# Kernel tuning notes

Measured on AMD Instinct MI355X. Metric: run time of the kernel, lower is better.

The kernel has to match this reference:

```python
import jax, jax.numpy as jnp
import numpy as np

B, L_IN, T = 1024, 512, 96
IN_DIM, OUT_DIM = 1, 1
H_ENC, H_DEC = 128, 256  # decoder hidden = 2 * encoder hidden (bidir concat)


def _lstm_cell(x, h, c, Wih, Whh, b):
    # PyTorch gate order: i, f, g, o. b = b_ih + b_hh (equivalent to two biases).
    gates = x @ Wih.T + h @ Whh.T + b
    i, f, g, o = jnp.split(gates, 4, axis=-1)
    c = jax.nn.sigmoid(f) * c + jax.nn.sigmoid(i) * jnp.tanh(g)
    h = jax.nn.sigmoid(o) * jnp.tanh(c)
    return h, c


def _lstm_final(xs, Wih, Whh, b, hidden, reverse=False):
    # xs: [L, B, D]; returns final (h, c) only (encoder outputs are unused).
    h0 = jnp.zeros((xs.shape[1], hidden), xs.dtype)
    c0 = jnp.zeros((xs.shape[1], hidden), xs.dtype)

    def step(carry, x):
        h, c = _lstm_cell(x, carry[0], carry[1], Wih, Whh, b)
        return (h, c), None

    (h, c), _ = jax.lax.scan(step, (h0, c0), xs, reverse=reverse)
    return h, c


def setup_inputs() -> dict:
    key = jax.random.key(0)
    ks = jax.random.split(key, 13)
    p = lambda k, s: (jax.random.normal(k, s, jnp.float32) * 0.05)
    return {
        "source": jax.random.normal(ks[0], (B, L_IN, IN_DIM), jnp.float32),
        "target_tensor": jnp.zeros((B, T, OUT_DIM), jnp.float32),
        "enc_Wih_f": p(ks[1], (4 * H_ENC, IN_DIM)),
        "enc_Whh_f": p(ks[2], (4 * H_ENC, H_ENC)),
        "enc_b_f": p(ks[3], (4 * H_ENC,)),
        "enc_Wih_b": p(ks[4], (4 * H_ENC, IN_DIM)),
        "enc_Whh_b": p(ks[5], (4 * H_ENC, H_ENC)),
        "enc_b_b": p(ks[6], (4 * H_ENC,)),
        "dec_Wih": p(ks[7], (4 * H_DEC, OUT_DIM)),
        "dec_Whh": p(ks[8], (4 * H_DEC, H_DEC)),
        "dec_b": p(ks[9], (4 * H_DEC,)),
        "out_W": p(ks[10], (OUT_DIM, H_DEC)),
        "out_b": p(ks[11], (OUT_DIM,)),
    }


def reference(source, target_tensor, enc_Wih_f, enc_Whh_f, enc_b_f,
              enc_Wih_b, enc_Whh_b, enc_b_b,
              dec_Wih, dec_Whh, dec_b, out_W, out_b):
    batch = source.shape[0]
    t_len = target_tensor.shape[1]
    out_dim = target_tensor.shape[-1]

    xs = jnp.swapaxes(source, 0, 1)  # [L, B, IN]
    h_f, c_f = _lstm_final(xs, enc_Wih_f, enc_Whh_f, enc_b_f, H_ENC, reverse=False)
    h_b, c_b = _lstm_final(xs, enc_Wih_b, enc_Whh_b, enc_b_b, H_ENC, reverse=True)
    h0 = jnp.concatenate([h_f, h_b], axis=-1)  # [B, 2*H_ENC]
    c0 = jnp.concatenate([c_f, c_b], axis=-1)

    y0 = jnp.zeros((batch, out_dim), source.dtype)

    def dec_step(carry, _):
        h, c, y = carry
        h, c = _lstm_cell(y, h, c, dec_Wih, dec_Whh, dec_b)
        y = h @ out_W.T + out_b
        return (h, c, y), y

    _, ys = jax.lax.scan(dec_step, (h0, c0, y0), None, length=t_len)
    return jnp.swapaxes(ys, 0, 1)  # [B, T, OUT]
```

## Files before the change

### kernel.cpp

```cpp
#include <hip/hip_runtime.h>
#include <math.h>

#define H_ENC 128
#define H_DEC 256
#define L_SRC 512
#define T_DEC 96
#define B_TOT 1024

typedef _Float16 half8 __attribute__((ext_vector_type(8)));
typedef float f32x4 __attribute__((ext_vector_type(4)));

#define MFMA16(A, B, C) __builtin_amdgcn_mfma_f32_16x16x32_f16((A), (B), (C), 0, 0, 0)

__device__ __forceinline__ unsigned packu(float a, float b) {
    union { _Float16 h[2]; unsigned u; } x; x.h[0] = (_Float16)a; x.h[1] = (_Float16)b; return x.u;
}

__device__ __forceinline__ float sigmoidf_(float x) {
    return __builtin_amdgcn_rcpf(1.f + __expf(-x));
}
__device__ __forceinline__ float tanhf_(float x) {
    return 1.f - 2.f * __builtin_amdgcn_rcpf(__expf(2.f * x) + 1.f);
}

#define CNT_STRIDE 104
__global__ void zero_cnt(int* cnt) {
    int i = blockIdx.x * blockDim.x + threadIdx.x;
    if (i < 64 * CNT_STRIDE) cnt[i] = 0;
}

#define EB 8
#define HPAD 136
__global__ __launch_bounds__(1024)
void encoder_big(
    const float* __restrict__ source,
    const float* __restrict__ Wih_f, const float* __restrict__ Whh_f, const float* __restrict__ b_f,
    const float* __restrict__ Wih_b, const float* __restrict__ Whh_b, const float* __restrict__ b_b,
    float* __restrict__ h0, float* __restrict__ c0)
{
    const int dir = blockIdx.x & 1;
    const int bg  = blockIdx.x >> 1;
    const int t   = threadIdx.x;
    const int w   = t >> 6;
    const int l   = t & 63;
    const int col = l & 15;
    const int grp = l >> 4;

    const float* Wih = dir ? Wih_b : Wih_f;
    const float* Whh = dir ? Whh_b : Whh_f;
    const float* bb  = dir ? b_b   : b_f;

    __shared__ float    xsT[L_SRC][EB];
    __shared__ _Float16 hbuf[2][16][HPAD];
    __shared__ float    gbuf[4][EB][H_ENC];

    {
        const float* srcb = source + (size_t)bg * EB * L_SRC;
        for (int i = t; i < EB * L_SRC; i += 1024) {
            int b = i >> 9, st = i & 511;
            xsT[st][b] = srcb[i];
        }
        for (int i = t; i < 2 * 16 * HPAD; i += 1024)
            ((_Float16*)hbuf)[i] = (_Float16)0.f;
    }

    half8 wf[2][4];
    #pragma unroll
    for (int tau = 0; tau < 2; ++tau) {
        const int n = 2 * w + tau;
        const int grow = (n >> 3) * H_ENC + 16 * (n & 7) + col;
        const float* wr = Whh + (size_t)grow * H_ENC;
        #pragma unroll
        for (int kt = 0; kt < 4; ++kt) {
            const float* p = wr + 32 * kt + 8 * grp;
            float4 v0 = *reinterpret_cast<const float4*>(p);
            float4 v1 = *reinterpret_cast<const float4*>(p + 4);
            half8 h;
            h[0] = (_Float16)v0.x; h[1] = (_Float16)v0.y; h[2] = (_Float16)v0.z; h[3] = (_Float16)v0.w;
            h[4] = (_Float16)v1.x; h[5] = (_Float16)v1.y; h[6] = (_Float16)v1.z; h[7] = (_Float16)v1.w;
            wf[tau][kt] = h;
        }
    }

    const int ub = t >> 7;
    const int ue = t & 127;
    const float bI = bb[ue],           wI = Wih[ue];
    const float bF = bb[H_ENC + ue],   wF = Wih[H_ENC + ue];
    const float bG = bb[2*H_ENC + ue], wG = Wih[2*H_ENC + ue];
    const float bO = bb[3*H_ENC + ue], wO = Wih[3*H_ENC + ue];

    float c = 0.f, hlast = 0.f;
    __syncthreads();

    int cur = 0;
    for (int s = 0; s < L_SRC; ++s) {
        const int step = dir ? (L_SRC - 1 - s) : s;

        half8 a0 = *reinterpret_cast<const half8*>(&hbuf[cur][col][ 0 + 8 * grp]);
        half8 a1 = *reinterpret_cast<const half8*>(&hbuf[cur][col][32 + 8 * grp]);
        half8 a2 = *reinterpret_cast<const half8*>(&hbuf[cur][col][64 + 8 * grp]);
        half8 a3 = *reinterpret_cast<const half8*>(&hbuf[cur][col][96 + 8 * grp]);

        f32x4 acc0 = {0.f, 0.f, 0.f, 0.f};
        f32x4 acc1 = {0.f, 0.f, 0.f, 0.f};
        acc0 = MFMA16(a0, wf[0][0], acc0); acc0 = MFMA16(a1, wf[0][1], acc0);
        acc0 = MFMA16(a2, wf[0][2], acc0); acc0 = MFMA16(a3, wf[0][3], acc0);
        acc1 = MFMA16(a0, wf[1][0], acc1); acc1 = MFMA16(a1, wf[1][1], acc1);
        acc1 = MFMA16(a2, wf[1][2], acc1); acc1 = MFMA16(a3, wf[1][3], acc1);

        if (grp < 2) {
            #pragma unroll
            for (int tau = 0; tau < 2; ++tau) {
                const int n = 2 * w + tau;
                const int G = n >> 3;
                const int e = 16 * (n & 7) + col;
                const f32x4 acc = tau ? acc1 : acc0;
                #pragma unroll
                for (int r = 0; r < 4; ++r)
                    gbuf[G][4 * grp + r][e] = acc[r];
            }
        }
        __syncthreads();

        {
            float x = xsT[step][ub];
            float gi = sigmoidf_(gbuf[0][ub][ue] + bI + wI * x);
            float gf = sigmoidf_(gbuf[1][ub][ue] + bF + wF * x);
            float gg = tanhf_  (gbuf[2][ub][ue] + bG + wG * x);
            float go = sigmoidf_(gbuf[3][ub][ue] + bO + wO * x);
            c = gf * c + gi * gg;
            float h = go * tanhf_(c);
            hlast = h;
            hbuf[cur ^ 1][ub][ue] = (_Float16)h;
        }
        __syncthreads();
        cur ^= 1;
    }

    h0[(size_t)(bg * EB + ub) * (2 * H_ENC) + dir * H_ENC + ue] = hlast;
    c0[(size_t)(bg * EB + ub) * (2 * H_ENC) + dir * H_ENC + ue] = c;
}

#define DB 16
__global__ __launch_bounds__(512, 2)
void decoder_split(
    const float* __restrict__ Wih,
    const float* __restrict__ bb,
    const float* __restrict__ outW,
    const float* __restrict__ outb,
    const float* __restrict__ h0,
    const float* __restrict__ c0,
    const float* __restrict__ Whh,
    unsigned* __restrict__ hx,
    int* __restrict__ cnt,
    float* __restrict__ out)
{
    const int blk = blockIdx.x;
    const int bg  = blk & 63;
    const int q   = blk >> 6;
    const int t   = threadIdx.x;
    const int w   = t >> 6;
    const int l   = t & 63;
    const int col = l & 15;
    const int grp = l >> 4;
    const int u   = w >> 1;
    const int fo  = w & 1;

    __shared__ unsigned hlU[DB][132];
    __shared__ float    exch[4][2][DB][16];
    __shared__ unsigned hnewU[DB][32];
    __shared__ float    yl[DB];
    __shared__ float    owl[H_DEC];
    int* mycnt = cnt + bg * CNT_STRIDE;

    if (t < H_DEC) owl[t] = outW[t];

    const int j0 = 64 * q + 16 * u + col;
    const int rA = (fo ? 256 : 0) + j0;
    const int rB = (fo ? 768 : 512) + j0;

    half8 wfA[8], wfB[8];
    #pragma unroll
    for (int kt = 0; kt < 8; ++kt) {
        const float* pa = Whh + (size_t)rA * H_DEC + 32 * kt + 8 * grp;
        const float* pb = Whh + (size_t)rB * H_DEC + 32 * kt + 8 * grp;
        float4 a0 = *reinterpret_cast<const float4*>(pa);
        float4 a1 = *reinterpret_cast<const float4*>(pa + 4);
        float4 b0 = *reinterpret_cast<const float4*>(pb);
        float4 b1 = *reinterpret_cast<const float4*>(pb + 4);
        half8 ha, hb;
        ha[0]=(_Float16)a0.x; ha[1]=(_Float16)a0.y; ha[2]=(_Float16)a0.z; ha[3]=(_Float16)a0.w;
        ha[4]=(_Float16)a1.x; ha[5]=(_Float16)a1.y; ha[6]=(_Float16)a1.z; ha[7]=(_Float16)a1.w;
        hb[0]=(_Float16)b0.x; hb[1]=(_Float16)b0.y; hb[2]=(_Float16)b0.z; hb[3]=(_Float16)b0.w;
        hb[4]=(_Float16)b1.x; hb[5]=(_Float16)b1.y; hb[6]=(_Float16)b1.z; hb[7]=(_Float16)b1.w;
        wfA[kt] = ha; wfB[kt] = hb;
    }

    const float bI = bb[j0],       wI = Wih[j0];
    const float bF = bb[256 + j0], wF = Wih[256 + j0];
    const float bG = bb[512 + j0], wG = Wih[512 + j0];
    const float bO = bb[768 + j0], wO = Wih[768 + j0];
    const float ob = outb[0];

    float c[4];
    #pragma unroll
    for (int r = 0; r < 4; ++r)
        c[r] = c0[(size_t)(bg * DB + 4 * grp + r) * H_DEC + j0];

    {
        int batch = t >> 5, pair = t & 31;
        int e = 64 * q + 2 * pair;
        const float* hp = h0 + (size_t)(bg * DB + batch) * H_DEC + e;
        unsigned v = packu(hp[0], hp[1]);
        __hip_atomic_store(&hx[(size_t)(bg * DB + batch) * 128 + 32 * q + pair], v,
                           __ATOMIC_RELAXED, __HIP_MEMORY_SCOPE_AGENT);
    }
    __syncthreads();
    if (t == 0) {
        __hip_atomic_fetch_add(&mycnt[0], 1, __ATOMIC_RELEASE, __HIP_MEMORY_SCOPE_AGENT);
        while (__hip_atomic_load(&mycnt[0], __ATOMIC_RELAXED, __HIP_MEMORY_SCOPE_AGENT) < 4) {}
    }
    __syncthreads();

    for (int s = 1; s <= T_DEC; ++s) {
        const int rb = (s - 1) & 1, wb = s & 1;
        #pragma unroll
        for (int i = 0; i < 4; ++i) {
            int j = t + 512 * i;
            int batch = j >> 7, within = j & 127;
            unsigned v = __hip_atomic_load(
                &hx[(size_t)rb * (B_TOT * 128) + (size_t)(bg * DB + batch) * 128 + within],
                __ATOMIC_RELAXED, __HIP_MEMORY_SCOPE_AGENT);
            hlU[batch][within] = v;
        }
        __syncthreads();

        {
            int batch = t >> 5, seg = t & 31;
            half8 hv = *reinterpret_cast<const half8*>(
                reinterpret_cast<const char*>(hlU) + batch * 528 + seg * 16);
            float sum = 0.f;
            #pragma unroll
            for (int j = 0; j < 8; ++j) sum += (float)hv[j] * owl[8 * seg + j];
            #pragma unroll
            for (int m = 1; m < 32; m <<= 1) sum += __shfl_xor(sum, m);
            if (seg == 0) {
                float yv = sum + ob;
                yl[batch] = (s == 1) ? 0.f : yv;
                if (q == 0 && s >= 2) out[(size_t)(bg * DB + batch) * T_DEC + (s - 2)] = yv;
            }
        }

        half8 a[8];
        #pragma unroll
        for (int kt = 0; kt < 8; ++kt)
            a[kt] = *reinterpret_cast<const half8*>(
                reinterpret_cast<const char*>(hlU) + col * 528 + (32 * kt + 8 * grp) * 2);

        f32x4 accA = {0.f, 0.f, 0.f, 0.f};
        f32x4 accB = {0.f, 0.f, 0.f, 0.f};
        #pragma unroll
        for (int kt = 0; kt < 8; ++kt) {
            accA = MFMA16(a[kt], wfA[kt], accA);
            accB = MFMA16(a[kt], wfB[kt], accB);
        }

        if (fo) {
            #pragma unroll
            for (int r = 0; r < 4; ++r) {
                exch[u][0][4 * grp + r][col] = accA[r] + bF;
                exch[u][1][4 * grp + r][col] = accB[r] + bO;
            }
        }
        __syncthreads();

        if (!fo) {
            #pragma unroll
            for (int r = 0; r < 4; ++r) {
                float yb = yl[4 * grp + r];
                float gi = sigmoidf_(accA[r] + bI + wI * yb);
                float gg = tanhf_  (accB[r] + bG + wG * yb);
                float gf = sigmoidf_(exch[u][0][4 * grp + r][col] + wF * yb);
                float go = sigmoidf_(exch[u][1][4 * grp + r][col] + wO * yb);
                c[r] = gf * c[r] + gi * gg;
                float h = go * tanhf_(c[r]);
                reinterpret_cast<_Float16*>(hnewU)[(4 * grp + r) * 64 + 16 * u + col] = (_Float16)h;
            }
        }
        __syncthreads();

        {
            int batch = t >> 5, pair = t & 31;
            __hip_atomic_store(
                &hx[(size_t)wb * (B_TOT * 128) + (size_t)(bg * DB + batch) * 128 + 32 * q + pair],
                hnewU[batch][pair], __ATOMIC_RELAXED, __HIP_MEMORY_SCOPE_AGENT);
        }
        __syncthreads();
        if (t == 0) {
            __hip_atomic_fetch_add(&mycnt[s], 1, __ATOMIC_RELEASE, __HIP_MEMORY_SCOPE_AGENT);
            while (__hip_atomic_load(&mycnt[s], __ATOMIC_RELAXED, __HIP_MEMORY_SCOPE_AGENT) < 4) {}
        }
        __syncthreads();
    }

    {
        #pragma unroll
        for (int i = 0; i < 4; ++i) {
            int j = t + 512 * i;
            int batch = j >> 7, within = j & 127;
            unsigned v = __hip_atomic_load(
                &hx[(size_t)(bg * DB + batch) * 128 + within],
                __ATOMIC_RELAXED, __HIP_MEMORY_SCOPE_AGENT);
            hlU[batch][within] = v;
        }
        __syncthreads();
        int batch = t >> 5, seg = t & 31;
        half8 hv = *reinterpret_cast<const half8*>(
            reinterpret_cast<const char*>(hlU) + batch * 528 + seg * 16);
        float sum = 0.f;
        #pragma unroll
        for (int j = 0; j < 8; ++j) sum += (float)hv[j] * owl[8 * seg + j];
        #pragma unroll
        for (int m = 1; m < 32; m <<= 1) sum += __shfl_xor(sum, m);
        if (q == 0 && seg == 0)
            out[(size_t)(bg * DB + batch) * T_DEC + (T_DEC - 1)] = sum + ob;
    }
}

extern "C" void kernel_launch(void* const* d_in, const int* in_sizes, int n_in,
                              void* d_out, int out_size, void* d_ws, size_t ws_size,
                              hipStream_t stream) {
    const float* source = (const float*)d_in[0];
    const float* eWih_f = (const float*)d_in[2];
    const float* eWhh_f = (const float*)d_in[3];
    const float* eb_f   = (const float*)d_in[4];
    const float* eWih_b = (const float*)d_in[5];
    const float* eWhh_b = (const float*)d_in[6];
    const float* eb_b   = (const float*)d_in[7];
    const float* dWih   = (const float*)d_in[8];
    const float* dWhh   = (const float*)d_in[9];
    const float* db     = (const float*)d_in[10];
    const float* oW     = (const float*)d_in[11];
    const float* obp    = (const float*)d_in[12];
    float* out = (float*)d_out;

    float*    h0  = (float*)d_ws;
    float*    c0  = h0 + (size_t)B_TOT * H_DEC;
    unsigned* hx  = (unsigned*)(c0 + (size_t)B_TOT * H_DEC);
    int*      cnt = (int*)(hx + (size_t)2 * B_TOT * 128);

    zero_cnt<<<(64 * CNT_STRIDE + 255) / 256, 256, 0, stream>>>(cnt);
    encoder_big<<<128 * 2, 1024, 0, stream>>>(
        source, eWih_f, eWhh_f, eb_f, eWih_b, eWhh_b, eb_b, h0, c0);
    decoder_split<<<256, 512, 0, stream>>>(
        dWih, db, oW, obp, h0, c0, dWhh, hx, cnt, out);
}
```

Measured before the change: 915.0 us.

## Shrink encoder h buffer, fold bias into MFMA, relax decoder barrier atomics

The encoder's LDS h buffer shrinks to the 8 real batch rows, with the padding rows fed as zeros. The gate bias now seeds the MFMA accumulators, which removes four adds per gate evaluation, and the MFMA block runs under raised wave priority. In the decoder's cross-block barrier, the arrive atomic drops from release to relaxed ordering and the spin loop gains s_sleep. That cuts fence cost and memory polling, but relaxed ordering may no longer guarantee that the hx stores are visible to the other blocks before the counter increments.

```diff
diff --git a/kernel.cpp b/kernel.cpp
--- a/kernel.cpp
+++ b/kernel.cpp
@@ -32,7 +32,7 @@
 #define EB 8
 #define HPAD 136
 __global__ __launch_bounds__(1024)
-void encoder_big(
+void encoder_eb8(
     const float* __restrict__ source,
     const float* __restrict__ Wih_f, const float* __restrict__ Whh_f, const float* __restrict__ b_f,
     const float* __restrict__ Wih_b, const float* __restrict__ Whh_b, const float* __restrict__ b_b,
@@ -51,7 +51,7 @@
     const float* bb  = dir ? b_b   : b_f;
 
     __shared__ float    xsT[L_SRC][EB];
-    __shared__ _Float16 hbuf[2][16][HPAD];
+    __shared__ _Float16 hbuf[2][EB][HPAD];
     __shared__ float    gbuf[4][EB][H_ENC];
 
     {
@@ -60,15 +60,17 @@
             int b = i >> 9, st = i & 511;
             xsT[st][b] = srcb[i];
         }
-        for (int i = t; i < 2 * 16 * HPAD; i += 1024)
+        for (int i = t; i < 2 * EB * HPAD; i += 1024)
             ((_Float16*)hbuf)[i] = (_Float16)0.f;
     }
 
     half8 wf[2][4];
+    float bias2[2];
     #pragma unroll
     for (int tau = 0; tau < 2; ++tau) {
         const int n = 2 * w + tau;
         const int grow = (n >> 3) * H_ENC + 16 * (n & 7) + col;
+        bias2[tau] = bb[grow];
         const float* wr = Whh + (size_t)grow * H_ENC;
         #pragma unroll
         for (int kt = 0; kt < 4; ++kt) {
@@ -84,10 +86,10 @@
 
     const int ub = t >> 7;
     const int ue = t & 127;
-    const float bI = bb[ue],           wI = Wih[ue];
-    const float bF = bb[H_ENC + ue],   wF = Wih[H_ENC + ue];
-    const float bG = bb[2*H_ENC + ue], wG = Wih[2*H_ENC + ue];
-    const float bO = bb[3*H_ENC + ue], wO = Wih[3*H_ENC + ue];
+    const float wI = Wih[ue];
+    const float wF = Wih[H_ENC + ue];
+    const float wG = Wih[2*H_ENC + ue];
+    const float wO = Wih[3*H_ENC + ue];
 
     float c = 0.f, hlast = 0.f;
     __syncthreads();
@@ -96,17 +98,22 @@
     for (int s = 0; s < L_SRC; ++s) {
         const int step = dir ? (L_SRC - 1 - s) : s;
 
-        half8 a0 = *reinterpret_cast<const half8*>(&hbuf[cur][col][ 0 + 8 * grp]);
-        half8 a1 = *reinterpret_cast<const half8*>(&hbuf[cur][col][32 + 8 * grp]);
-        half8 a2 = *reinterpret_cast<const half8*>(&hbuf[cur][col][64 + 8 * grp]);
-        half8 a3 = *reinterpret_cast<const half8*>(&hbuf[cur][col][96 + 8 * grp]);
-
-        f32x4 acc0 = {0.f, 0.f, 0.f, 0.f};
-        f32x4 acc1 = {0.f, 0.f, 0.f, 0.f};
+        half8 a0 = {0,0,0,0,0,0,0,0}, a1 = a0, a2 = a0, a3 = a0;
+        if (col < EB) {
+            a0 = *reinterpret_cast<const half8*>(&hbuf[cur][col][ 0 + 8 * grp]);
+            a1 = *reinterpret_cast<const half8*>(&hbuf[cur][col][32 + 8 * grp]);
+            a2 = *reinterpret_cast<const half8*>(&hbuf[cur][col][64 + 8 * grp]);
+            a3 = *reinterpret_cast<const half8*>(&hbuf[cur][col][96 + 8 * grp]);
+        }
+
+        f32x4 acc0 = {bias2[0], bias2[0], bias2[0], bias2[0]};
+        f32x4 acc1 = {bias2[1], bias2[1], bias2[1], bias2[1]};
+        __builtin_amdgcn_s_setprio(1);
         acc0 = MFMA16(a0, wf[0][0], acc0); acc0 = MFMA16(a1, wf[0][1], acc0);
         acc0 = MFMA16(a2, wf[0][2], acc0); acc0 = MFMA16(a3, wf[0][3], acc0);
         acc1 = MFMA16(a0, wf[1][0], acc1); acc1 = MFMA16(a1, wf[1][1], acc1);
         acc1 = MFMA16(a2, wf[1][2], acc1); acc1 = MFMA16(a3, wf[1][3], acc1);
+        __builtin_amdgcn_s_setprio(0);
 
         if (grp < 2) {
             #pragma unroll
@@ -124,10 +131,10 @@
 
         {
             float x = xsT[step][ub];
-            float gi = sigmoidf_(gbuf[0][ub][ue] + bI + wI * x);
-            float gf = sigmoidf_(gbuf[1][ub][ue] + bF + wF * x);
-            float gg = tanhf_  (gbuf[2][ub][ue] + bG + wG * x);
-            float go = sigmoidf_(gbuf[3][ub][ue] + bO + wO * x);
+            float gi = sigmoidf_(gbuf[0][ub][ue] + wI * x);
+            float gf = sigmoidf_(gbuf[1][ub][ue] + wF * x);
+            float gg = tanhf_  (gbuf[2][ub][ue] + wG * x);
+            float go = sigmoidf_(gbuf[3][ub][ue] + wO * x);
             c = gf * c + gi * gg;
             float h = go * tanhf_(c);
             hlast = h;
@@ -217,8 +224,9 @@
     }
     __syncthreads();
     if (t == 0) {
-        __hip_atomic_fetch_add(&mycnt[0], 1, __ATOMIC_RELEASE, __HIP_MEMORY_SCOPE_AGENT);
-        while (__hip_atomic_load(&mycnt[0], __ATOMIC_RELAXED, __HIP_MEMORY_SCOPE_AGENT) < 4) {}
+        __hip_atomic_fetch_add(&mycnt[0], 1, __ATOMIC_RELAXED, __HIP_MEMORY_SCOPE_AGENT);
+        while (__hip_atomic_load(&mycnt[0], __ATOMIC_RELAXED, __HIP_MEMORY_SCOPE_AGENT) < 4)
+            __builtin_amdgcn_s_sleep(1);
     }
     __syncthreads();
 
@@ -297,8 +305,9 @@
         }
         __syncthreads();
         if (t == 0) {
-            __hip_atomic_fetch_add(&mycnt[s], 1, __ATOMIC_RELEASE, __HIP_MEMORY_SCOPE_AGENT);
-            while (__hip_atomic_load(&mycnt[s], __ATOMIC_RELAXED, __HIP_MEMORY_SCOPE_AGENT) < 4) {}
+            __hip_atomic_fetch_add(&mycnt[s], 1, __ATOMIC_RELAXED, __HIP_MEMORY_SCOPE_AGENT);
+            while (__hip_atomic_load(&mycnt[s], __ATOMIC_RELAXED, __HIP_MEMORY_SCOPE_AGENT) < 4)
+                __builtin_amdgcn_s_sleep(1);
         }
         __syncthreads();
     }
@@ -350,7 +359,7 @@
     int*      cnt = (int*)(hx + (size_t)2 * B_TOT * 128);
 
     zero_cnt<<<(64 * CNT_STRIDE + 255) / 256, 256, 0, stream>>>(cnt);
-    encoder_big<<<128 * 2, 1024, 0, stream>>>(
+    encoder_eb8<<<128 * 2, 1024, 0, stream>>>(
         source, eWih_f, eWhh_f, eb_f, eWih_b, eWhh_b, eb_b, h0, c0);
     decoder_split<<<256, 512, 0, stream>>>(
         dWih, db, oW, obp, h0, c0, dWhh, hx, cnt, out);
```

After: 771.2 us. -15.7%, faster.
